# Performance work log

Measured on AMD Instinct MI355X. Metric: run time of the kernel, lower is better.

## Reference

```python
import jax, jax.numpy as jnp
import numpy as np

N = 2048
D_T = 256; D_F = 256
E_T = 32; E_F = 32; E_C = 128
C = 5; Q = 512


def setup_inputs() -> dict:
    key = jax.random.key(0)
    ks = jax.random.split(key, 12)
    # full graph minus self-loops, row-major (matches dense_to_sparse ordering)
    r, c = np.meshgrid(np.arange(N), np.arange(N), indexing='ij')
    m = r != c
    edge_index = jnp.asarray(np.stack([r[m], c[m]]), dtype=jnp.int32)  # [2, N*(N-1)]
    E = edge_index.shape[1]
    s = 0.02
    return {
        'time_features': jax.random.normal(ks[0], (N, D_T), jnp.float32),
        'edge_index': edge_index,
        'time_edge_weight': jax.random.uniform(ks[1], (E,), jnp.float32),
        'freq_features': jax.random.normal(ks[2], (N, D_F), jnp.float32),
        'freq_edge_weight': jax.random.uniform(ks[3], (E,), jnp.float32),
        'labels': jax.random.randint(ks[4], (N,), 0, C, jnp.int32),
        'num_classes': C,
        'query_size': Q,
        'Wt': jax.random.normal(ks[5], (D_T, E_T), jnp.float32) * s,
        'bt': jnp.zeros((E_T,), jnp.float32),
        'Wf': jax.random.normal(ks[6], (D_F, E_F), jnp.float32) * s,
        'bf': jnp.zeros((E_F,), jnp.float32),
        'Wc': jax.random.normal(ks[7], (E_T + E_F + C, E_C), jnp.float32) * s,
        'bc': jnp.zeros((E_C,), jnp.float32),
        'Wo': jax.random.normal(ks[8], (E_C, C), jnp.float32) * s,
        'bo': jnp.zeros((C,), jnp.float32),
    }


def _gcn(x, A, W, b):
    # torch_geometric GCNConv: D^{-1/2}(A + I)D^{-1/2} (X W) + b
    n = A.shape[0]
    Ah = A + jnp.eye(n, dtype=A.dtype)
    deg = Ah.sum(axis=1)
    dis = jnp.where(deg > 0, jax.lax.rsqrt(deg), 0.0)
    return (dis[:, None] * Ah * dis[None, :]) @ (x @ W) + b


def reference(time_features, edge_index, time_edge_weight, freq_features,
              freq_edge_weight, labels, num_classes, query_size,
              Wt, bt, Wf, bf, Wc, bc, Wo, bo):
    n = time_features.shape[0]
    lrelu = lambda z: jax.nn.leaky_relu(z, 0.01)

    def dense_adj(w):  # A[dst, src] = w
        return jnp.zeros((n, n), w.dtype).at[edge_index[1], edge_index[0]].add(w)

    te = lrelu(_gcn(time_features, dense_adj(time_edge_weight), Wt, bt))
    fe = lrelu(_gcn(freq_features, dense_adj(freq_edge_weight), Wf, bf))

    # to_one_hot: one_hot[:n - query_size, labels] = 1 -> support rows get 1 in
    # every column that appears anywhere in `labels`
    cols = jnp.zeros((num_classes,), te.dtype).at[labels].set(1.0)
    rowmask = (jnp.arange(n) < (n - query_size)).astype(te.dtype)
    one_hot = rowmask[:, None] * cols[None, :]

    feats = jnp.concatenate([te, fe, one_hot], axis=-1)  # [n, E_T+E_F+C]

    # graph_construction (no_grad in original): 1 / (L1 distance over the
    # non-one-hot dims + 1e-5), zero diagonal
    fd = jax.lax.stop_gradient(feats[:, : feats.shape[1] - num_classes])
    dist = jnp.sum(jnp.abs(fd[:, None, :] - fd[None, :, :]), axis=-1)  # [n, n]
    Aw = (1.0 / (dist + 1e-5)) * (1.0 - jnp.eye(n, dtype=feats.dtype))

    emb = lrelu(_gcn(feats, Aw, Wc, bc))
    return emb @ Wo + bo
```

## Files before the change

kernel.cpp:

```cpp
#include <hip/hip_runtime.h>
#include <hip/hip_bf16.h>

#define N 2048
#define NM1 2047
#define DT 256
#define ET 32
#define EC 128
#define NC 5
#define FS 80
#define FD 69
#define KC_ET 16
#define KC_EC 16

typedef __hip_bfloat16 bf16;
typedef unsigned short u16;
typedef float f32x4 __attribute__((ext_vector_type(4)));
typedef __bf16 bf16x8 __attribute__((ext_vector_type(8)));

__device__ inline u16 bf16_rne(float x){
    unsigned int b = __float_as_uint(x);
    b += 0x7fffu + ((b >> 16) & 1u);
    return (u16)(b >> 16);
}
__device__ inline float bf16_to_f(u16 h){
    return __uint_as_float(((unsigned int)h) << 16);
}

__device__ inline f32x4 mfma16x16x32(bf16x8 a, bf16x8 b, f32x4 c){
    return __builtin_amdgcn_mfma_f32_16x16x32_bf16(a, b, c, 0, 0, 0);
}

__global__ __launch_bounds__(256) void k_deg_label_xw(const float* __restrict__ tw,
                                                      const float* __restrict__ fw,
                                                      const int* __restrict__ labels,
                                                      const float* __restrict__ Xt,
                                                      const float* __restrict__ Wt,
                                                      const float* __restrict__ Xf,
                                                      const float* __restrict__ Wf,
                                                      float* __restrict__ degT,
                                                      float* __restrict__ degF,
                                                      float* __restrict__ cols,
                                                      float* __restrict__ Yt,
                                                      float* __restrict__ Yf){
    int b = blockIdx.x;
    int t = threadIdx.x;
    if (b < 512){
        int p = (b & 7)*256 + t;
        if (p >= NM1) return;
        int s0 = (b >> 3)*32;
        float lowT=0.f, highT=0.f, lowF=0.f, highF=0.f;
        #pragma unroll 8
        for (int r = 0; r < 32; ++r){
            int s = s0 + r;
            float vt = tw[(size_t)s*NM1 + p];
            float vf = fw[(size_t)s*NM1 + p];
            if (s <= p){ highT += vt; highF += vf; }
            else       { lowT  += vt; lowF  += vf; }
        }
        atomicAdd(&degT[p],   lowT);
        atomicAdd(&degF[p],   lowF);
        atomicAdd(&degT[p+1], highT);
        atomicAdd(&degF[p+1], highF);
        return;
    }
    if (b == 512){
        __shared__ float lc[NC];
        if (t < NC) lc[t] = 0.f;
        __syncthreads();
        for (int i = t; i < N; i += 256){
            int l = labels[i];
            if (l >= 0 && l < NC) lc[l] = 1.f;
        }
        __syncthreads();
        if (t < NC) cols[t] = lc[t];
        return;
    }
    int idx = b - 513;
    const float* X = (idx & 256) ? Xf : Xt;
    const float* W = (idx & 256) ? Wf : Wt;
    float*       Y = (idx & 256) ? Yf : Yt;
    __shared__ float Ws[DT*ET];
    __shared__ float Xs[8*DT];
    for (int j = t; j < DT*ET; j += 256) Ws[j] = W[j];
    int i0 = (idx & 255)*8;
    for (int j = t; j < 8*DT; j += 256) Xs[j] = X[(size_t)i0*DT + j];
    __syncthreads();
    int r = t >> 5, f = t & 31;
    const float* xr = Xs + r*DT;
    float acc = 0.f;
    #pragma unroll 8
    for (int d = 0; d < DT; ++d) acc += xr[d]*Ws[d*ET+f];
    Y[(size_t)(i0+r)*ET+f] = acc;
}

__global__ __launch_bounds__(256) void k_agg_et(const float* __restrict__ tw,
                                                const float* __restrict__ fw,
                                                const float* __restrict__ Yt,
                                                const float* __restrict__ Yf,
                                                const float* __restrict__ degT,
                                                const float* __restrict__ degF,
                                                float* __restrict__ Pt,
                                                float* __restrict__ Pf){
    __shared__ float Ast[64*68];
    __shared__ float Asf[64*68];
    __shared__ float Zst[64*ET];
    __shared__ float Zsf[64*ET];
    int t = threadIdx.x;
    int i0 = blockIdx.x*64;
    int kc = blockIdx.y;
    int k0 = kc*128;
    int g  = t >> 7;
    int tt = t & 127;
    int ig = tt >> 3, fg = tt & 7;
    int r0 = ig*4, c0 = fg*4;
    const float* As = g ? Asf : Ast;
    const float* Zs = g ? Zsf : Zst;
    float acc[4][4];
    #pragma unroll
    for (int u=0;u<4;++u)
        #pragma unroll
        for (int v=0;v<4;++v) acc[u][v]=0.f;

    for (int kt = 0; kt < 2; ++kt){
        int kb = k0 + kt*64;
        #pragma unroll
        for (int e = 0; e < 16; ++e){
            int id = t + e*256;
            int k_l = id >> 6, i_l = id & 63;
            int k = kb + k_l;
            int gi = i0 + i_l;
            float vt, vf;
            if (gi == k){ vt = 0.f; vf = 0.f; }
            else {
                size_t base = (size_t)k*NM1 + gi - (gi > k ? 1 : 0);
                vt = tw[base]; vf = fw[base];
            }
            Ast[k_l*68 + i_l] = vt;
            Asf[k_l*68 + i_l] = vf;
        }
        #pragma unroll
        for (int e = 0; e < 2; ++e){
            int id = t + e*256;
            int row = id >> 3;
            int c4  = (id & 7)*4;
            float rdT = rsqrtf(1.f + degT[kb+row]);
            float rdF = rsqrtf(1.f + degF[kb+row]);
            float4 yt = *(const float4*)&Yt[(size_t)(kb+row)*ET + c4];
            float4 yf = *(const float4*)&Yf[(size_t)(kb+row)*ET + c4];
            yt.x*=rdT; yt.y*=rdT; yt.z*=rdT; yt.w*=rdT;
            yf.x*=rdF; yf.y*=rdF; yf.z*=rdF; yf.w*=rdF;
            *(float4*)&Zst[row*ET + c4] = yt;
            *(float4*)&Zsf[row*ET + c4] = yf;
        }
        __syncthreads();
        for (int k = 0; k < 64; ++k){
            float4 a = *(const float4*)&As[k*68 + r0];
            float4 z = *(const float4*)&Zs[k*ET + c0];
            const float* ap = (const float*)&a;
            const float* zp = (const float*)&z;
            #pragma unroll
            for (int u = 0; u < 4; ++u)
                #pragma unroll
                for (int v = 0; v < 4; ++v)
                    acc[u][v] += ap[u]*zp[v];
        }
        __syncthreads();
    }
    float* P = g ? Pf : Pt;
    #pragma unroll
    for (int u = 0; u < 4; ++u){
        size_t ii = (size_t)(i0 + r0 + u);
        float4 o;
        float* po = (float*)&o;
        #pragma unroll
        for (int v = 0; v < 4; ++v) po[v]=acc[u][v];
        *(float4*)&P[(size_t)kc*(N*ET) + ii*ET + c0] = o;
    }
}

__global__ __launch_bounds__(256) void k_feats_epi(const float* __restrict__ Pt,
                                                   const float* __restrict__ Pf,
                                                   const float* __restrict__ Yt,
                                                   const float* __restrict__ Yf,
                                                   const float* __restrict__ degT,
                                                   const float* __restrict__ degF,
                                                   const float* __restrict__ bt,
                                                   const float* __restrict__ bfv,
                                                   const float* __restrict__ cols,
                                                   const int* __restrict__ qsize,
                                                   float* __restrict__ feats){
    int idx = blockIdx.x*256 + threadIdx.x;
    int i = idx >> 6;
    int f = idx & 63;
    float s, rd, b;
    if (f < ET){
        rd = rsqrtf(1.f + degT[i]);
        s = rd*Yt[(size_t)i*ET + f];
        #pragma unroll
        for (int kc = 0; kc < KC_ET; ++kc) s += Pt[(size_t)kc*(N*ET) + (size_t)i*ET + f];
        b = bt[f];
    } else {
        int g = f - ET;
        rd = rsqrtf(1.f + degF[i]);
        s = rd*Yf[(size_t)i*ET + g];
        #pragma unroll
        for (int kc = 0; kc < KC_ET; ++kc) s += Pf[(size_t)kc*(N*ET) + (size_t)i*ET + g];
        b = bfv[g];
    }
    float v = rd*s + b;
    feats[(size_t)i*FS + f] = v > 0.f ? v : 0.01f*v;
    if (f < NC){
        int nsup = N - qsize[0];
        feats[(size_t)i*FS + 2*ET + f] = (i < nsup) ? cols[f] : 0.f;
    }
}

__global__ __launch_bounds__(256) void k_build_aw(const float* __restrict__ feats,
                                                  u16* __restrict__ Aw_hi,
                                                  u16* __restrict__ Aw_lo,
                                                  float* __restrict__ dsum){
    __shared__ float fiT[64*68];
    __shared__ float fjT[64*68];
    int t = threadIdx.x;
    int i0 = blockIdx.x*64, j0 = blockIdx.y*64;
    {
        int row = t >> 2;
        int cb  = (t & 3)*16;
        const float4* si = (const float4*)(feats + (size_t)(i0+row)*FS + cb);
        const float4* sj = (const float4*)(feats + (size_t)(j0+row)*FS + cb);
        #pragma unroll
        for (int s = 0; s < 4; ++s){
            float4 v = si[s];
            float4 w = sj[s];
            int c = cb + s*4;
            fiT[(c+0)*68+row]=v.x; fiT[(c+1)*68+row]=v.y; fiT[(c+2)*68+row]=v.z; fiT[(c+3)*68+row]=v.w;
            fjT[(c+0)*68+row]=w.x; fjT[(c+1)*68+row]=w.y; fjT[(c+2)*68+row]=w.z; fjT[(c+3)*68+row]=w.w;
        }
    }
    __syncthreads();
    int tx = t & 15, ty = t >> 4;
    float acc[4][4];
    #pragma unroll
    for (int u=0;u<4;++u)
        #pragma unroll
        for (int v=0;v<4;++v) acc[u][v]=0.f;
    for (int d = 0; d < 64; ++d){
        float4 a4 = *(const float4*)&fiT[d*68 + ty*4];
        float4 b4 = *(const float4*)&fjT[d*68 + tx*4];
        const float* ap = (const float*)&a4;
        const float* bp = (const float*)&b4;
        #pragma unroll
        for (int u = 0; u < 4; ++u)
            #pragma unroll
            for (int v = 0; v < 4; ++v)
                acc[u][v] += fabsf(ap[u]-bp[v]);
    }
    #pragma unroll
    for (int u = 0; u < 4; ++u){
        int gi = i0 + ty*4 + u;
        float po[4];
        u16 hh[4], ll[4];
        #pragma unroll
        for (int v = 0; v < 4; ++v){
            int gj = j0 + tx*4 + v;
            float w = (gi==gj) ? 1.0f : 1.0f/(acc[u][v] + 1e-5f);
            po[v] = w;
            u16 h = bf16_rne(w);
            hh[v] = h;
            ll[v] = bf16_rne(w - bf16_to_f(h));
        }
        uint2 ph, pl;
        ph.x = (unsigned)hh[0] | ((unsigned)hh[1]<<16);
        ph.y = (unsigned)hh[2] | ((unsigned)hh[3]<<16);
        pl.x = (unsigned)ll[0] | ((unsigned)ll[1]<<16);
        pl.y = (unsigned)ll[2] | ((unsigned)ll[3]<<16);
        *(uint2*)&Aw_hi[(size_t)gi*N + j0 + tx*4] = ph;
        *(uint2*)&Aw_lo[(size_t)gi*N + j0 + tx*4] = pl;
        float rs = (po[0]+po[1]) + (po[2]+po[3]);
        rs += __shfl_xor(rs, 1);
        rs += __shfl_xor(rs, 2);
        rs += __shfl_xor(rs, 4);
        rs += __shfl_xor(rs, 8);
        if (tx == 0) atomicAdd(&dsum[gi], rs);
    }
}

__global__ __launch_bounds__(256) void k_featswc(const float* __restrict__ feats,
                                                 const float* __restrict__ Wc,
                                                 const float* __restrict__ dsum,
                                                 u16* __restrict__ ZcT_hi,
                                                 u16* __restrict__ ZcT_lo){
    __shared__ float Wcs[FD*EC];
    __shared__ float fr[8][FD+3];
    __shared__ float zb[128][12];
    int t = threadIdx.x;
    for (int idx = t; idx < FD*EC; idx += 256) Wcs[idx] = Wc[idx];
    int i0 = blockIdx.x*8;
    for (int idx = t; idx < 8*FD; idx += 256){
        int r = idx / FD;
        int c = idx - r*FD;
        fr[r][c] = feats[(size_t)(i0+r)*FS + c];
    }
    __syncthreads();
    int f  = t & 127;
    int rh = t >> 7;
    for (int rr = 0; rr < 4; ++rr){
        int r = rh*4 + rr;
        float acc = 0.f;
        #pragma unroll
        for (int d = 0; d < FD; ++d) acc += fr[r][d]*Wcs[d*EC+f];
        int i = i0 + r;
        zb[f][r] = rsqrtf(dsum[i])*acc;
    }
    __syncthreads();
    int p = rh, f2 = f;
    float4 v0 = *(const float4*)&zb[f2][0];
    float4 v1 = *(const float4*)&zb[f2][4];
    float vv[8] = {v0.x, v0.y, v0.z, v0.w, v1.x, v1.y, v1.z, v1.w};
    u16 s[8];
    #pragma unroll
    for (int j = 0; j < 8; ++j){
        u16 h = bf16_rne(vv[j]);
        s[j] = p ? bf16_rne(vv[j] - bf16_to_f(h)) : h;
    }
    uint4 pk;
    pk.x = (unsigned)s[0] | ((unsigned)s[1]<<16);
    pk.y = (unsigned)s[2] | ((unsigned)s[3]<<16);
    pk.z = (unsigned)s[4] | ((unsigned)s[5]<<16);
    pk.w = (unsigned)s[6] | ((unsigned)s[7]<<16);
    u16* dst = p ? ZcT_lo : ZcT_hi;
    *(uint4*)&dst[(size_t)f2*N + i0] = pk;
}

__global__ __launch_bounds__(256) void k_agg_ec(const u16* __restrict__ Aw_hi,
                                                const u16* __restrict__ Aw_lo,
                                                const u16* __restrict__ ZcT_hi,
                                                const u16* __restrict__ ZcT_lo,
                                                float* __restrict__ Pe){
    __shared__ u16 Ah[64*72];
    __shared__ u16 Al[64*72];
    __shared__ u16 Zh[128*72];
    __shared__ u16 Zl[128*72];
    int t = threadIdx.x;
    int w  = t >> 6;
    int l  = t & 63;
    int lr = l & 15;
    int lg = l >> 4;
    int i0 = blockIdx.x*64;
    int kb0 = blockIdx.y*128;
    f32x4 acc[8];
    #pragma unroll
    for (int tt = 0; tt < 8; ++tt) acc[tt] = (f32x4){0.f, 0.f, 0.f, 0.f};

    for (int sub = 0; sub < 2; ++sub){
        int kbs = kb0 + sub*64;
        #pragma unroll
        for (int e = 0; e < 2; ++e){
            int id = t + e*256;
            int row = id >> 3, ch = (id & 7)*8;
            uint4 vh = *(const uint4*)&Aw_hi[(size_t)(i0+row)*N + kbs + ch];
            uint4 vl = *(const uint4*)&Aw_lo[(size_t)(i0+row)*N + kbs + ch];
            *(uint4*)&Ah[row*72 + ch] = vh;
            *(uint4*)&Al[row*72 + ch] = vl;
        }
        #pragma unroll
        for (int e = 0; e < 4; ++e){
            int id = t + e*256;
            int row = id >> 3, ch = (id & 7)*8;
            uint4 vh = *(const uint4*)&ZcT_hi[(size_t)row*N + kbs + ch];
            uint4 vl = *(const uint4*)&ZcT_lo[(size_t)row*N + kbs + ch];
            *(uint4*)&Zh[row*72 + ch] = vh;
            *(uint4*)&Zl[row*72 + ch] = vl;
        }
        __syncthreads();
        #pragma unroll
        for (int ks = 0; ks < 2; ++ks){
            int aoff = (w*16 + lr)*72 + ks*32 + lg*8;
            bf16x8 aH = *(const bf16x8*)&Ah[aoff];
            bf16x8 aL = *(const bf16x8*)&Al[aoff];
            #pragma unroll
            for (int tt = 0; tt < 8; ++tt){
                int zoff = (tt*16 + lr)*72 + ks*32 + lg*8;
                bf16x8 bH = *(const bf16x8*)&Zh[zoff];
                bf16x8 bL = *(const bf16x8*)&Zl[zoff];
                acc[tt] = mfma16x16x32(aH, bH, acc[tt]);
                acc[tt] = mfma16x16x32(aL, bH, acc[tt]);
                acc[tt] = mfma16x16x32(aH, bL, acc[tt]);
            }
        }
        __syncthreads();
    }
    float* pout = Pe + (size_t)blockIdx.y*((size_t)N*EC);
    #pragma unroll
    for (int tt = 0; tt < 8; ++tt){
        #pragma unroll
        for (int r = 0; r < 4; ++r){
            int gi = i0 + w*16 + lg*4 + r;
            pout[(size_t)gi*EC + tt*16 + lr] = acc[tt][r];
        }
    }
}

__global__ __launch_bounds__(256) void k_embfinal(const float* __restrict__ Pe,
                                                  const float* __restrict__ dsum,
                                                  const float* __restrict__ bc,
                                                  const float* __restrict__ Wo,
                                                  const float* __restrict__ bo,
                                                  float* __restrict__ out){
    __shared__ float vs[2][EC];
    __shared__ float Wos[EC*NC];
    __shared__ float bos[NC];
    int t = threadIdx.x;
    for (int idx = t; idx < EC*NC; idx += 256) Wos[idx] = Wo[idx];
    if (t < NC) bos[t] = bo[t];
    int rr = t >> 7, f = t & 127;
    int i = blockIdx.x*2 + rr;
    size_t idx = (size_t)i*EC + f;
    float s = 0.f;
    #pragma unroll
    for (int kc = 0; kc < KC_EC; ++kc) s += Pe[(size_t)kc*(N*EC) + idx];
    float v = rsqrtf(dsum[i])*s + bc[f];
    vs[rr][f] = v > 0.f ? v : 0.01f*v;
    __syncthreads();
    if (t < 2*NC){
        int r = t / NC;
        int c = t - r*NC;
        float a = bos[c];
        #pragma unroll 8
        for (int f2 = 0; f2 < EC; ++f2) a += vs[r][f2]*Wos[f2*NC+c];
        out[(size_t)(blockIdx.x*2 + r)*NC + c] = a;
    }
}

extern "C" void kernel_launch(void* const* d_in, const int* in_sizes, int n_in,
                              void* d_out, int out_size, void* d_ws, size_t ws_size,
                              hipStream_t stream) {
    const float* time_features = (const float*)d_in[0];
    const float* tw            = (const float*)d_in[2];
    const float* freq_features = (const float*)d_in[3];
    const float* fw            = (const float*)d_in[4];
    const int*   labels        = (const int*)d_in[5];
    const int*   qsize         = (const int*)d_in[7];
    const float* Wt  = (const float*)d_in[8];
    const float* bt  = (const float*)d_in[9];
    const float* Wf  = (const float*)d_in[10];
    const float* bfv = (const float*)d_in[11];
    const float* Wc  = (const float*)d_in[12];
    const float* bc  = (const float*)d_in[13];
    const float* Wo  = (const float*)d_in[14];
    const float* bo  = (const float*)d_in[15];
    float* out = (float*)d_out;

    float* ws    = (float*)d_ws;
    float* Yt    = ws;
    float* Yf    = Yt + (size_t)N*ET;
    float* Zc    = Yf + (size_t)N*ET;
    float* degT  = Zc + (size_t)N*EC;
    float* degF  = degT + N;
    float* dsum  = degF + N;
    float* colsb = dsum + N;
    float* feats = colsb + 8;
    float* Aw    = feats + (size_t)N*FS;
    float* Pt    = Aw + (size_t)N*N;
    float* Pf    = Pt + (size_t)KC_ET*N*ET;
    float* Pe    = Pf + (size_t)KC_ET*N*ET;

    u16* Aw_hi  = (u16*)Aw;
    u16* Aw_lo  = Aw_hi + (size_t)N*N;
    u16* ZcT_hi = (u16*)Zc;
    u16* ZcT_lo = ZcT_hi + (size_t)N*EC;

    hipMemsetAsync(degT, 0, 3*N*sizeof(float), stream);
    k_deg_label_xw<<<1025, 256, 0, stream>>>(tw, fw, labels,
                                             time_features, Wt, freq_features, Wf,
                                             degT, degF, colsb, Yt, Yf);
    k_agg_et<<<dim3(N/64, KC_ET), 256, 0, stream>>>(tw, fw, Yt, Yf, degT, degF, Pt, Pf);
    k_feats_epi<<<(N*64)/256, 256, 0, stream>>>(Pt, Pf, Yt, Yf, degT, degF,
                                                bt, bfv, colsb, qsize, feats);
    k_build_aw<<<dim3(N/64, N/64), 256, 0, stream>>>(feats, Aw_hi, Aw_lo, dsum);
    k_featswc<<<N/8, 256, 0, stream>>>(feats, Wc, dsum, ZcT_hi, ZcT_lo);
    k_agg_ec<<<dim3(N/64, KC_EC), 256, 0, stream>>>(Aw_hi, Aw_lo, ZcT_hi, ZcT_lo, Pe);
    k_embfinal<<<N/2, 256, 0, stream>>>(Pe, dsum, bc, Wo, bo, out);
}
```

Measured before the change: 199.8 us.

## Fuse all stages into one persistent cooperative kernel with grid syncs

```diff
diff --git a/kernel.cpp b/kernel.cpp
--- a/kernel.cpp
+++ b/kernel.cpp
@@ -1,5 +1,8 @@
 #include <hip/hip_runtime.h>
 #include <hip/hip_bf16.h>
+#include <hip/hip_cooperative_groups.h>
+
+namespace cg = cooperative_groups;
 
 #define N 2048
 #define NM1 2047
@@ -11,8 +14,8 @@
 #define FD 69
 #define KC_ET 16
 #define KC_EC 16
-
-typedef __hip_bfloat16 bf16;
+#define SMEM_MAX 55296
+
 typedef unsigned short u16;
 typedef float f32x4 __attribute__((ext_vector_type(4)));
 typedef __bf16 bf16x8 __attribute__((ext_vector_type(8)));
@@ -25,89 +28,81 @@
 __device__ inline float bf16_to_f(u16 h){
     return __uint_as_float(((unsigned int)h) << 16);
 }
-
 __device__ inline f32x4 mfma16x16x32(bf16x8 a, bf16x8 b, f32x4 c){
     return __builtin_amdgcn_mfma_f32_16x16x32_bf16(a, b, c, 0, 0, 0);
 }
 
-__global__ __launch_bounds__(256) void k_deg_label_xw(const float* __restrict__ tw,
-                                                      const float* __restrict__ fw,
-                                                      const int* __restrict__ labels,
-                                                      const float* __restrict__ Xt,
-                                                      const float* __restrict__ Wt,
-                                                      const float* __restrict__ Xf,
-                                                      const float* __restrict__ Wf,
-                                                      float* __restrict__ degT,
-                                                      float* __restrict__ degF,
-                                                      float* __restrict__ cols,
-                                                      float* __restrict__ Yt,
-                                                      float* __restrict__ Yf){
-    int b = blockIdx.x;
-    int t = threadIdx.x;
-    if (b < 512){
-        int p = (b & 7)*256 + t;
-        if (p >= NM1) return;
-        int s0 = (b >> 3)*32;
-        float lowT=0.f, highT=0.f, lowF=0.f, highF=0.f;
+struct Params {
+    const float* tw; const float* fw;
+    const int* labels; const int* qsize;
+    const float* Xt; const float* Wt; const float* Xf; const float* Wf;
+    const float* bt; const float* bfv;
+    const float* Wc; const float* bc; const float* Wo; const float* bo;
+    float* degT; float* degF; float* dsum; float* colsb;
+    float* Yt; float* Yf; float* feats;
+    u16* Aw_hi; u16* Aw_lo; u16* ZcT_hi; u16* ZcT_lo;
+    float* Pt; float* Pf; float* Pe;
+    float* out;
+};
+
+__device__ inline void ph_deg_label_xw(int vb, char* smem, const Params& P){
+    int t = threadIdx.x;
+    if (vb < 512){
+        int p = (vb & 7)*256 + t;
+        if (p < NM1){
+            int s0 = (vb >> 3)*32;
+            float lowT=0.f, highT=0.f, lowF=0.f, highF=0.f;
+            #pragma unroll 8
+            for (int r = 0; r < 32; ++r){
+                int s = s0 + r;
+                float vt = P.tw[(size_t)s*NM1 + p];
+                float vf = P.fw[(size_t)s*NM1 + p];
+                if (s <= p){ highT += vt; highF += vf; }
+                else       { lowT  += vt; lowF  += vf; }
+            }
+            atomicAdd(&P.degT[p],   lowT);
+            atomicAdd(&P.degF[p],   lowF);
+            atomicAdd(&P.degT[p+1], highT);
+            atomicAdd(&P.degF[p+1], highF);
+        }
+    } else if (vb == 512){
+        float* lc = (float*)smem;
+        __syncthreads();
+        if (t < NC) lc[t] = 0.f;
+        __syncthreads();
+        for (int i = t; i < N; i += 256){
+            int l = P.labels[i];
+            if (l >= 0 && l < NC) lc[l] = 1.f;
+        }
+        __syncthreads();
+        if (t < NC) P.colsb[t] = lc[t];
+    } else {
+        int idx = vb - 513;
+        const float* X = (idx & 256) ? P.Xf : P.Xt;
+        const float* W = (idx & 256) ? P.Wf : P.Wt;
+        float*       Y = (idx & 256) ? P.Yf : P.Yt;
+        float* Ws = (float*)smem;
+        float* Xs = Ws + DT*ET;
+        __syncthreads();
+        for (int j = t; j < DT*ET; j += 256) Ws[j] = W[j];
+        int i0 = (idx & 255)*8;
+        for (int j = t; j < 8*DT; j += 256) Xs[j] = X[(size_t)i0*DT + j];
+        __syncthreads();
+        int r = t >> 5, f = t & 31;
+        const float* xr = Xs + r*DT;
+        float acc = 0.f;
         #pragma unroll 8
-        for (int r = 0; r < 32; ++r){
-            int s = s0 + r;
-            float vt = tw[(size_t)s*NM1 + p];
-            float vf = fw[(size_t)s*NM1 + p];
-            if (s <= p){ highT += vt; highF += vf; }
-            else       { lowT  += vt; lowF  += vf; }
-        }
-        atomicAdd(&degT[p],   lowT);
-        atomicAdd(&degF[p],   lowF);
-        atomicAdd(&degT[p+1], highT);
-        atomicAdd(&degF[p+1], highF);
-        return;
-    }
-    if (b == 512){
-        __shared__ float lc[NC];
-        if (t < NC) lc[t] = 0.f;
-        __syncthreads();
-        for (int i = t; i < N; i += 256){
-            int l = labels[i];
-            if (l >= 0 && l < NC) lc[l] = 1.f;
-        }
-        __syncthreads();
-        if (t < NC) cols[t] = lc[t];
-        return;
-    }
-    int idx = b - 513;
-    const float* X = (idx & 256) ? Xf : Xt;
-    const float* W = (idx & 256) ? Wf : Wt;
-    float*       Y = (idx & 256) ? Yf : Yt;
-    __shared__ float Ws[DT*ET];
-    __shared__ float Xs[8*DT];
-    for (int j = t; j < DT*ET; j += 256) Ws[j] = W[j];
-    int i0 = (idx & 255)*8;
-    for (int j = t; j < 8*DT; j += 256) Xs[j] = X[(size_t)i0*DT + j];
-    __syncthreads();
-    int r = t >> 5, f = t & 31;
-    const float* xr = Xs + r*DT;
-    float acc = 0.f;
-    #pragma unroll 8
-    for (int d = 0; d < DT; ++d) acc += xr[d]*Ws[d*ET+f];
-    Y[(size_t)(i0+r)*ET+f] = acc;
-}
-
-__global__ __launch_bounds__(256) void k_agg_et(const float* __restrict__ tw,
-                                                const float* __restrict__ fw,
-                                                const float* __restrict__ Yt,
-                                                const float* __restrict__ Yf,
-                                                const float* __restrict__ degT,
-                                                const float* __restrict__ degF,
-                                                float* __restrict__ Pt,
-                                                float* __restrict__ Pf){
-    __shared__ float Ast[64*68];
-    __shared__ float Asf[64*68];
-    __shared__ float Zst[64*ET];
-    __shared__ float Zsf[64*ET];
-    int t = threadIdx.x;
-    int i0 = blockIdx.x*64;
-    int kc = blockIdx.y;
+        for (int d = 0; d < DT; ++d) acc += xr[d]*Ws[d*ET+f];
+        Y[(size_t)(i0+r)*ET+f] = acc;
+    }
+}
+
+__device__ inline void ph_agg_et(int i0, int kc, char* smem, const Params& P){
+    float* Ast = (float*)smem;
+    float* Asf = Ast + 64*68;
+    float* Zst = Asf + 64*68;
+    float* Zsf = Zst + 64*ET;
+    int t = threadIdx.x;
     int k0 = kc*128;
     int g  = t >> 7;
     int tt = t & 127;
@@ -133,7 +128,7 @@
             if (gi == k){ vt = 0.f; vf = 0.f; }
             else {
                 size_t base = (size_t)k*NM1 + gi - (gi > k ? 1 : 0);
-                vt = tw[base]; vf = fw[base];
+                vt = P.tw[base]; vf = P.fw[base];
             }
             Ast[k_l*68 + i_l] = vt;
             Asf[k_l*68 + i_l] = vf;
@@ -143,10 +138,10 @@
             int id = t + e*256;
             int row = id >> 3;
             int c4  = (id & 7)*4;
-            float rdT = rsqrtf(1.f + degT[kb+row]);
-            float rdF = rsqrtf(1.f + degF[kb+row]);
-            float4 yt = *(const float4*)&Yt[(size_t)(kb+row)*ET + c4];
-            float4 yf = *(const float4*)&Yf[(size_t)(kb+row)*ET + c4];
+            float rdT = rsqrtf(1.f + P.degT[kb+row]);
+            float rdF = rsqrtf(1.f + P.degF[kb+row]);
+            float4 yt = *(const float4*)&P.Yt[(size_t)(kb+row)*ET + c4];
+            float4 yf = *(const float4*)&P.Yf[(size_t)(kb+row)*ET + c4];
             yt.x*=rdT; yt.y*=rdT; yt.z*=rdT; yt.w*=rdT;
             yf.x*=rdF; yf.y*=rdF; yf.z*=rdF; yf.w*=rdF;
             *(float4*)&Zst[row*ET + c4] = yt;
@@ -166,7 +161,7 @@
         }
         __syncthreads();
     }
-    float* P = g ? Pf : Pt;
+    float* Pp = g ? P.Pf : P.Pt;
     #pragma unroll
     for (int u = 0; u < 4; ++u){
         size_t ii = (size_t)(i0 + r0 + u);
@@ -174,60 +169,47 @@
         float* po = (float*)&o;
         #pragma unroll
         for (int v = 0; v < 4; ++v) po[v]=acc[u][v];
-        *(float4*)&P[(size_t)kc*(N*ET) + ii*ET + c0] = o;
-    }
-}
-
-__global__ __launch_bounds__(256) void k_feats_epi(const float* __restrict__ Pt,
-                                                   const float* __restrict__ Pf,
-                                                   const float* __restrict__ Yt,
-                                                   const float* __restrict__ Yf,
-                                                   const float* __restrict__ degT,
-                                                   const float* __restrict__ degF,
-                                                   const float* __restrict__ bt,
-                                                   const float* __restrict__ bfv,
-                                                   const float* __restrict__ cols,
-                                                   const int* __restrict__ qsize,
-                                                   float* __restrict__ feats){
-    int idx = blockIdx.x*256 + threadIdx.x;
+        *(float4*)&Pp[(size_t)kc*(N*ET) + ii*ET + c0] = o;
+    }
+}
+
+__device__ inline void ph_feats_epi(int vb, const Params& P){
+    int idx = vb*256 + (int)threadIdx.x;
     int i = idx >> 6;
     int f = idx & 63;
     float s, rd, b;
     if (f < ET){
-        rd = rsqrtf(1.f + degT[i]);
-        s = rd*Yt[(size_t)i*ET + f];
-        #pragma unroll
-        for (int kc = 0; kc < KC_ET; ++kc) s += Pt[(size_t)kc*(N*ET) + (size_t)i*ET + f];
-        b = bt[f];
+        rd = rsqrtf(1.f + P.degT[i]);
+        s = rd*P.Yt[(size_t)i*ET + f];
+        #pragma unroll
+        for (int kc = 0; kc < KC_ET; ++kc) s += P.Pt[(size_t)kc*(N*ET) + (size_t)i*ET + f];
+        b = P.bt[f];
     } else {
         int g = f - ET;
-        rd = rsqrtf(1.f + degF[i]);
-        s = rd*Yf[(size_t)i*ET + g];
-        #pragma unroll
-        for (int kc = 0; kc < KC_ET; ++kc) s += Pf[(size_t)kc*(N*ET) + (size_t)i*ET + g];
-        b = bfv[g];
+        rd = rsqrtf(1.f + P.degF[i]);
+        s = rd*P.Yf[(size_t)i*ET + g];
+        #pragma unroll
+        for (int kc = 0; kc < KC_ET; ++kc) s += P.Pf[(size_t)kc*(N*ET) + (size_t)i*ET + g];
+        b = P.bfv[g];
     }
     float v = rd*s + b;
-    feats[(size_t)i*FS + f] = v > 0.f ? v : 0.01f*v;
+    P.feats[(size_t)i*FS + f] = v > 0.f ? v : 0.01f*v;
     if (f < NC){
-        int nsup = N - qsize[0];
-        feats[(size_t)i*FS + 2*ET + f] = (i < nsup) ? cols[f] : 0.f;
-    }
-}
-
-__global__ __launch_bounds__(256) void k_build_aw(const float* __restrict__ feats,
-                                                  u16* __restrict__ Aw_hi,
-                                                  u16* __restrict__ Aw_lo,
-                                                  float* __restrict__ dsum){
-    __shared__ float fiT[64*68];
-    __shared__ float fjT[64*68];
-    int t = threadIdx.x;
-    int i0 = blockIdx.x*64, j0 = blockIdx.y*64;
+        int nsup = N - P.qsize[0];
+        P.feats[(size_t)i*FS + 2*ET + f] = (i < nsup) ? P.colsb[f] : 0.f;
+    }
+}
+
+__device__ inline void ph_build_aw(int i0, int j0, char* smem, const Params& P){
+    float* fiT = (float*)smem;
+    float* fjT = fiT + 64*68;
+    int t = threadIdx.x;
+    __syncthreads();
     {
         int row = t >> 2;
         int cb  = (t & 3)*16;
-        const float4* si = (const float4*)(feats + (size_t)(i0+row)*FS + cb);
-        const float4* sj = (const float4*)(feats + (size_t)(j0+row)*FS + cb);
+        const float4* si = (const float4*)(P.feats + (size_t)(i0+row)*FS + cb);
+        const float4* sj = (const float4*)(P.feats + (size_t)(j0+row)*FS + cb);
         #pragma unroll
         for (int s = 0; s < 4; ++s){
             float4 v = si[s];
@@ -274,32 +256,33 @@
         ph.y = (unsigned)hh[2] | ((unsigned)hh[3]<<16);
         pl.x = (unsigned)ll[0] | ((unsigned)ll[1]<<16);
         pl.y = (unsigned)ll[2] | ((unsigned)ll[3]<<16);
-        *(uint2*)&Aw_hi[(size_t)gi*N + j0 + tx*4] = ph;
-        *(uint2*)&Aw_lo[(size_t)gi*N + j0 + tx*4] = pl;
+        *(uint2*)&P.Aw_hi[(size_t)gi*N + j0 + tx*4] = ph;
+        *(uint2*)&P.Aw_lo[(size_t)gi*N + j0 + tx*4] = pl;
         float rs = (po[0]+po[1]) + (po[2]+po[3]);
         rs += __shfl_xor(rs, 1);
         rs += __shfl_xor(rs, 2);
         rs += __shfl_xor(rs, 4);
         rs += __shfl_xor(rs, 8);
-        if (tx == 0) atomicAdd(&dsum[gi], rs);
-    }
-}
-
-__global__ __launch_bounds__(256) void k_featswc(const float* __restrict__ feats,
-                                                 const float* __restrict__ Wc,
-                                                 const float* __restrict__ dsum,
-                                                 u16* __restrict__ ZcT_hi,
-                                                 u16* __restrict__ ZcT_lo){
-    __shared__ float Wcs[FD*EC];
-    __shared__ float fr[8][FD+3];
-    __shared__ float zb[128][12];
-    int t = threadIdx.x;
-    for (int idx = t; idx < FD*EC; idx += 256) Wcs[idx] = Wc[idx];
-    int i0 = blockIdx.x*8;
+        if (tx == 0) atomicAdd(&P.dsum[gi], rs);
+    }
+}
+
+__device__ inline void ph_featswc_stage(char* smem, const Params& P){
+    float* Wcs = (float*)smem;
+    int t = threadIdx.x;
+    for (int idx = t; idx < FD*EC; idx += 256) Wcs[idx] = P.Wc[idx];
+}
+__device__ inline void ph_featswc(int vb, char* smem, const Params& P){
+    float* Wcs = (float*)smem;
+    float* fr  = Wcs + FD*EC;
+    float* zb  = fr + 8*72;
+    int t = threadIdx.x;
+    int i0 = vb*8;
+    __syncthreads();
     for (int idx = t; idx < 8*FD; idx += 256){
         int r = idx / FD;
         int c = idx - r*FD;
-        fr[r][c] = feats[(size_t)(i0+r)*FS + c];
+        fr[r*72 + c] = P.feats[(size_t)(i0+r)*FS + c];
     }
     __syncthreads();
     int f  = t & 127;
@@ -308,14 +291,14 @@
         int r = rh*4 + rr;
         float acc = 0.f;
         #pragma unroll
-        for (int d = 0; d < FD; ++d) acc += fr[r][d]*Wcs[d*EC+f];
+        for (int d = 0; d < FD; ++d) acc += fr[r*72+d]*Wcs[d*EC+f];
         int i = i0 + r;
-        zb[f][r] = rsqrtf(dsum[i])*acc;
+        zb[f*12 + r] = rsqrtf(P.dsum[i])*acc;
     }
     __syncthreads();
     int p = rh, f2 = f;
-    float4 v0 = *(const float4*)&zb[f2][0];
-    float4 v1 = *(const float4*)&zb[f2][4];
+    float4 v0 = *(const float4*)&zb[f2*12 + 0];
+    float4 v1 = *(const float4*)&zb[f2*12 + 4];
     float vv[8] = {v0.x, v0.y, v0.z, v0.w, v1.x, v1.y, v1.z, v1.w};
     u16 s[8];
     #pragma unroll
@@ -328,26 +311,22 @@
     pk.y = (unsigned)s[2] | ((unsigned)s[3]<<16);
     pk.z = (unsigned)s[4] | ((unsigned)s[5]<<16);
     pk.w = (unsigned)s[6] | ((unsigned)s[7]<<16);
-    u16* dst = p ? ZcT_lo : ZcT_hi;
+    u16* dst = p ? P.ZcT_lo : P.ZcT_hi;
     *(uint4*)&dst[(size_t)f2*N + i0] = pk;
 }
 
-__global__ __launch_bounds__(256) void k_agg_ec(const u16* __restrict__ Aw_hi,
-                                                const u16* __restrict__ Aw_lo,
-                                                const u16* __restrict__ ZcT_hi,
-                                                const u16* __restrict__ ZcT_lo,
-                                                float* __restrict__ Pe){
-    __shared__ u16 Ah[64*72];
-    __shared__ u16 Al[64*72];
-    __shared__ u16 Zh[128*72];
-    __shared__ u16 Zl[128*72];
+__device__ inline void ph_agg_ec(int ib, int kc, char* smem, const Params& P){
+    u16* Ah = (u16*)smem;
+    u16* Al = Ah + 64*72;
+    u16* Zh = Al + 64*72;
+    u16* Zl = Zh + 128*72;
     int t = threadIdx.x;
     int w  = t >> 6;
     int l  = t & 63;
     int lr = l & 15;
     int lg = l >> 4;
-    int i0 = blockIdx.x*64;
-    int kb0 = blockIdx.y*128;
+    int i0 = ib*64;
+    int kb0 = kc*128;
     f32x4 acc[8];
     #pragma unroll
     for (int tt = 0; tt < 8; ++tt) acc[tt] = (f32x4){0.f, 0.f, 0.f, 0.f};
@@ -358,8 +337,8 @@
         for (int e = 0; e < 2; ++e){
             int id = t + e*256;
             int row = id >> 3, ch = (id & 7)*8;
-            uint4 vh = *(const uint4*)&Aw_hi[(size_t)(i0+row)*N + kbs + ch];
-            uint4 vl = *(const uint4*)&Aw_lo[(size_t)(i0+row)*N + kbs + ch];
+            uint4 vh = *(const uint4*)&P.Aw_hi[(size_t)(i0+row)*N + kbs + ch];
+            uint4 vl = *(const uint4*)&P.Aw_lo[(size_t)(i0+row)*N + kbs + ch];
             *(uint4*)&Ah[row*72 + ch] = vh;
             *(uint4*)&Al[row*72 + ch] = vl;
         }
@@ -367,8 +346,8 @@
         for (int e = 0; e < 4; ++e){
             int id = t + e*256;
             int row = id >> 3, ch = (id & 7)*8;
-            uint4 vh = *(const uint4*)&ZcT_hi[(size_t)row*N + kbs + ch];
-            uint4 vl = *(const uint4*)&ZcT_lo[(size_t)row*N + kbs + ch];
+            uint4 vh = *(const uint4*)&P.ZcT_hi[(size_t)row*N + kbs + ch];
+            uint4 vl = *(const uint4*)&P.ZcT_lo[(size_t)row*N + kbs + ch];
             *(uint4*)&Zh[row*72 + ch] = vh;
             *(uint4*)&Zl[row*72 + ch] = vl;
         }
@@ -390,7 +369,7 @@
         }
         __syncthreads();
     }
-    float* pout = Pe + (size_t)blockIdx.y*((size_t)N*EC);
+    float* pout = P.Pe + (size_t)kc*((size_t)N*EC);
     #pragma unroll
     for (int tt = 0; tt < 8; ++tt){
         #pragma unroll
@@ -401,84 +380,163 @@
     }
 }
 
-__global__ __launch_bounds__(256) void k_embfinal(const float* __restrict__ Pe,
-                                                  const float* __restrict__ dsum,
-                                                  const float* __restrict__ bc,
-                                                  const float* __restrict__ Wo,
-                                                  const float* __restrict__ bo,
-                                                  float* __restrict__ out){
-    __shared__ float vs[2][EC];
-    __shared__ float Wos[EC*NC];
-    __shared__ float bos[NC];
-    int t = threadIdx.x;
-    for (int idx = t; idx < EC*NC; idx += 256) Wos[idx] = Wo[idx];
-    if (t < NC) bos[t] = bo[t];
+__device__ inline void ph_embfinal_stage(char* smem, const Params& P){
+    float* vs  = (float*)smem;
+    float* Wos = vs + 2*EC;
+    float* bos = Wos + EC*NC;
+    int t = threadIdx.x;
+    for (int idx = t; idx < EC*NC; idx += 256) Wos[idx] = P.Wo[idx];
+    if (t < NC) bos[t] = P.bo[t];
+}
+__device__ inline void ph_embfinal(int vb, char* smem, const Params& P){
+    float* vs  = (float*)smem;
+    float* Wos = vs + 2*EC;
+    float* bos = Wos + EC*NC;
+    int t = threadIdx.x;
+    __syncthreads();
     int rr = t >> 7, f = t & 127;
-    int i = blockIdx.x*2 + rr;
+    int i = vb*2 + rr;
     size_t idx = (size_t)i*EC + f;
     float s = 0.f;
     #pragma unroll
-    for (int kc = 0; kc < KC_EC; ++kc) s += Pe[(size_t)kc*(N*EC) + idx];
-    float v = rsqrtf(dsum[i])*s + bc[f];
-    vs[rr][f] = v > 0.f ? v : 0.01f*v;
+    for (int kc = 0; kc < KC_EC; ++kc) s += P.Pe[(size_t)kc*(N*EC) + idx];
+    float v = rsqrtf(P.dsum[i])*s + P.bc[f];
+    vs[rr*EC + f] = v > 0.f ? v : 0.01f*v;
     __syncthreads();
     if (t < 2*NC){
         int r = t / NC;
         int c = t - r*NC;
         float a = bos[c];
         #pragma unroll 8
-        for (int f2 = 0; f2 < EC; ++f2) a += vs[r][f2]*Wos[f2*NC+c];
-        out[(size_t)(blockIdx.x*2 + r)*NC + c] = a;
-    }
+        for (int f2 = 0; f2 < EC; ++f2) a += vs[r*EC + f2]*Wos[f2*NC+c];
+        P.out[(size_t)(vb*2 + r)*NC + c] = a;
+    }
+}
+
+__global__ __launch_bounds__(256, 2) void kfull(Params P){
+    __shared__ __align__(16) char smem[SMEM_MAX];
+    cg::grid_group grid = cg::this_grid();
+    int G = gridDim.x;
+    int b = blockIdx.x;
+    int t = threadIdx.x;
+
+    for (int idx = b*256 + t; idx < 3*N + 8; idx += G*256) P.degT[idx] = 0.f;
+    grid.sync();
+    for (int vb = b; vb < 1025; vb += G) ph_deg_label_xw(vb, smem, P);
+    grid.sync();
+    for (int vb = b; vb < 512; vb += G) ph_agg_et((vb & 31)*64, vb >> 5, smem, P);
+    grid.sync();
+    for (int vb = b; vb < 512; vb += G) ph_feats_epi(vb, P);
+    grid.sync();
+    for (int vb = b; vb < 1024; vb += G) ph_build_aw((vb & 31)*64, (vb >> 5)*64, smem, P);
+    grid.sync();
+    ph_featswc_stage(smem, P);
+    for (int vb = b; vb < 256; vb += G) ph_featswc(vb, smem, P);
+    grid.sync();
+    for (int vb = b; vb < 512; vb += G) ph_agg_ec(vb & 31, vb >> 5, smem, P);
+    grid.sync();
+    ph_embfinal_stage(smem, P);
+    for (int vb = b; vb < 1024; vb += G) ph_embfinal(vb, smem, P);
+}
+
+__global__ __launch_bounds__(256) void k1s(Params P){
+    __shared__ __align__(16) char s[(DT*ET + 8*DT)*4];
+    ph_deg_label_xw(blockIdx.x, s, P);
+}
+__global__ __launch_bounds__(256) void k2s(Params P){
+    __shared__ __align__(16) char s[(2*64*68 + 2*64*ET)*4];
+    ph_agg_et(((int)blockIdx.x & 31)*64, (int)blockIdx.x >> 5, s, P);
+}
+__global__ __launch_bounds__(256) void k3s(Params P){ ph_feats_epi(blockIdx.x, P); }
+__global__ __launch_bounds__(256) void k4s(Params P){
+    __shared__ __align__(16) char s[2*64*68*4];
+    ph_build_aw(((int)blockIdx.x & 31)*64, ((int)blockIdx.x >> 5)*64, s, P);
+}
+__global__ __launch_bounds__(256) void k5s(Params P){
+    __shared__ __align__(16) char s[(FD*EC + 8*72 + 128*12)*4];
+    ph_featswc_stage(s, P);
+    ph_featswc(blockIdx.x, s, P);
+}
+__global__ __launch_bounds__(256) void k6s(Params P){
+    __shared__ __align__(16) char s[SMEM_MAX];
+    ph_agg_ec((int)blockIdx.x & 31, (int)blockIdx.x >> 5, s, P);
+}
+__global__ __launch_bounds__(256) void k7s(Params P){
+    __shared__ __align__(16) char s[(2*EC + EC*NC + 8)*4];
+    ph_embfinal_stage(s, P);
+    ph_embfinal(blockIdx.x, s, P);
 }
 
 extern "C" void kernel_launch(void* const* d_in, const int* in_sizes, int n_in,
                               void* d_out, int out_size, void* d_ws, size_t ws_size,
                               hipStream_t stream) {
-    const float* time_features = (const float*)d_in[0];
-    const float* tw            = (const float*)d_in[2];
-    const float* freq_features = (const float*)d_in[3];
-    const float* fw            = (const float*)d_in[4];
-    const int*   labels        = (const int*)d_in[5];
-    const int*   qsize         = (const int*)d_in[7];
-    const float* Wt  = (const float*)d_in[8];
-    const float* bt  = (const float*)d_in[9];
-    const float* Wf  = (const float*)d_in[10];
-    const float* bfv = (const float*)d_in[11];
-    const float* Wc  = (const float*)d_in[12];
-    const float* bc  = (const float*)d_in[13];
-    const float* Wo  = (const float*)d_in[14];
-    const float* bo  = (const float*)d_in[15];
-    float* out = (float*)d_out;
+    Params P;
+    P.Xt     = (const float*)d_in[0];
+    P.tw     = (const float*)d_in[2];
+    P.Xf     = (const float*)d_in[3];
+    P.fw     = (const float*)d_in[4];
+    P.labels = (const int*)d_in[5];
+    P.qsize  = (const int*)d_in[7];
+    P.Wt  = (const float*)d_in[8];
+    P.bt  = (const float*)d_in[9];
+    P.Wf  = (const float*)d_in[10];
+    P.bfv = (const float*)d_in[11];
+    P.Wc  = (const float*)d_in[12];
+    P.bc  = (const float*)d_in[13];
+    P.Wo  = (const float*)d_in[14];
+    P.bo  = (const float*)d_in[15];
+    P.out = (float*)d_out;
 
     float* ws    = (float*)d_ws;
-    float* Yt    = ws;
-    float* Yf    = Yt + (size_t)N*ET;
-    float* Zc    = Yf + (size_t)N*ET;
-    float* degT  = Zc + (size_t)N*EC;
-    float* degF  = degT + N;
-    float* dsum  = degF + N;
-    float* colsb = dsum + N;
-    float* feats = colsb + 8;
-    float* Aw    = feats + (size_t)N*FS;
-    float* Pt    = Aw + (size_t)N*N;
-    float* Pf    = Pt + (size_t)KC_ET*N*ET;
-    float* Pe    = Pf + (size_t)KC_ET*N*ET;
-
-    u16* Aw_hi  = (u16*)Aw;
-    u16* Aw_lo  = Aw_hi + (size_t)N*N;
-    u16* ZcT_hi = (u16*)Zc;
-    u16* ZcT_lo = ZcT_hi + (size_t)N*EC;
-
-    hipMemsetAsync(degT, 0, 3*N*sizeof(float), stream);
-    k_deg_label_xw<<<1025, 256, 0, stream>>>(tw, fw, labels,
-                                             time_features, Wt, freq_features, Wf,
-                                             degT, degF, colsb, Yt, Yf);
-    k_agg_et<<<dim3(N/64, KC_ET), 256, 0, stream>>>(tw, fw, Yt, Yf, degT, degF, Pt, Pf);
-    k_feats_epi<<<(N*64)/256, 256, 0, stream>>>(Pt, Pf, Yt, Yf, degT, degF,
-                                                bt, bfv, colsb, qsize, feats);
-    k_build_aw<<<dim3(N/64, N/64), 256, 0, stream>>>(feats, Aw_hi, Aw_lo, dsum);
-    k_featswc<<<N/8, 256, 0, stream>>>(feats, Wc, dsum, ZcT_hi, ZcT_lo);
-    k_agg_ec<<<dim3(N/64, KC_EC), 256, 0, stream>>>(Aw_hi, Aw_lo, ZcT_hi, ZcT_lo, Pe);
-    k_embfinal<<<N/2, 256, 0, stream>>>(Pe, dsum, bc, Wo, bo, out);
-}
+    P.Yt    = ws;
+    P.Yf    = P.Yt + (size_t)N*ET;
+    float* Zc = P.Yf + (size_t)N*ET;
+    P.degT  = Zc + (size_t)N*EC;
+    P.degF  = P.degT + N;
+    P.dsum  = P.degF + N;
+    P.colsb = P.dsum + N;
+    P.feats = P.colsb + 8;
+    float* Aw = P.feats + (size_t)N*FS;
+    P.Pt    = Aw + (size_t)N*N;
+    P.Pf    = P.Pt + (size_t)KC_ET*N*ET;
+    P.Pe    = P.Pf + (size_t)KC_ET*N*ET;
+
+    P.Aw_hi  = (u16*)Aw;
+    P.Aw_lo  = P.Aw_hi + (size_t)N*N;
+    P.ZcT_hi = (u16*)Zc;
+    P.ZcT_lo = P.ZcT_hi + (size_t)N*EC;
+
+    static int gmax = 0;
+    if (gmax == 0){
+        int nb = 0;
+        if (hipOccupancyMaxActiveBlocksPerMultiprocessor(&nb, (const void*)kfull, 256, 0) != hipSuccess || nb < 1)
+            nb = 2;
+        int ncu = 0;
+        hipDeviceProp_t prop;
+        int dev = 0;
+        if (hipGetDevice(&dev) == hipSuccess && hipGetDeviceProperties(&prop, dev) == hipSuccess)
+            ncu = prop.multiProcessorCount;
+        if (ncu <= 0) ncu = 256;
+        long cap = (long)nb * (long)ncu;
+        gmax = cap < 512 ? (int)cap : 512;
+        if (gmax < 1) gmax = 1;
+    }
+
+    static int coop_ok = -1;
+    if (coop_ok != 0){
+        void* kargs[] = { (void*)&P };
+        hipError_t e = hipLaunchCooperativeKernel((const void*)kfull, dim3(gmax), dim3(256),
+                                                  kargs, 0, stream);
+        if (e == hipSuccess){ coop_ok = 1; return; }
+        coop_ok = 0;
+        (void)hipGetLastError();
+    }
+    hipMemsetAsync(P.degT, 0, (3*N + 8)*sizeof(float), stream);
+    k1s<<<1025, 256, 0, stream>>>(P);
+    k2s<<<512, 256, 0, stream>>>(P);
+    k3s<<<512, 256, 0, stream>>>(P);
+    k4s<<<1024, 256, 0, stream>>>(P);
+    k5s<<<256, 256, 0, stream>>>(P);
+    k6s<<<512, 256, 0, stream>>>(P);
+    k7s<<<1024, 256, 0, stream>>>(P);
+}
```

New measurement: 473.5 us. 137% more time.
